# Optimization experiments

Measured on AMD Instinct MI355X. Metric: run time of the kernel, lower is better.

The kernel has to match this reference:

```python
import jax, jax.numpy as jnp
import numpy as np

N_NODES = 100000


def _gcn_layer(x, src, dst, W, b, num_nodes):
    # Linear transform first (PyG GCNConv applies Linear before propagate).
    h = x @ W.T  # [N, out]
    # Degree (with self loops already included in src/dst), computed on target.
    ones = jnp.ones(dst.shape[0], dtype=h.dtype)
    deg = jax.ops.segment_sum(ones, dst, num_segments=num_nodes)
    dinv = jnp.where(deg > 0, jax.lax.rsqrt(deg), 0.0)
    norm = dinv[src] * dinv[dst]  # [E]
    msg = h[src] * norm[:, None]  # gather + per-edge scale, [E, out]
    out = jax.ops.segment_sum(msg, dst, num_segments=num_nodes)
    return out + b


def setup_inputs() -> dict:
    key = jax.random.key(0)
    k1, k2, k3, k4, k5, k6 = jax.random.split(key, 6)
    d = 64
    x = jax.random.normal(k1, (N_NODES, d), dtype=jnp.float32)
    edge_index = jax.random.randint(k2, (2, 1600000), 0, N_NODES, dtype=jnp.int64)
    s = 1.0 / np.sqrt(d)
    W1 = jax.random.normal(k3, (d, d), dtype=jnp.float32) * s
    b1 = jax.random.normal(k4, (d,), dtype=jnp.float32) * 0.01
    W2 = jax.random.normal(k5, (d, d), dtype=jnp.float32) * s
    b2 = jax.random.normal(k6, (d,), dtype=jnp.float32) * 0.01
    return {"x": x, "edge_index": edge_index, "W1": W1, "b1": b1, "W2": W2, "b2": b2}


def reference(x, edge_index, W1, b1, W2, b2):
    n = x.shape[0]
    loop = jnp.arange(n, dtype=edge_index.dtype)
    src = jnp.concatenate([edge_index[0], loop])  # add self loops
    dst = jnp.concatenate([edge_index[1], loop])
    h = _gcn_layer(x, src, dst, W1, b1, n)
    out = _gcn_layer(h, src, dst, W2, b2, n)
    return out
```

## Files before the change

kernel.cpp:

```cpp
#include <hip/hip_runtime.h>
#include <hip/hip_fp16.h>


#define D 64
#define NPB 128
#define MAXB 784
#define CHUNK 8192

__global__ __launch_bounds__(256) void hist_kernel(const int* __restrict__ dst,
                                                   int* __restrict__ counts,
                                                   int* __restrict__ cursor,
                                                   int nE, int B) {
    __shared__ int hist[MAXB];
    if (blockIdx.x == 0 && threadIdx.x == 0) *cursor = 0;
    int c = blockIdx.x;
    for (int b = threadIdx.x; b < B; b += 256) hist[b] = 0;
    __syncthreads();
    int e0 = c * CHUNK;
#pragma unroll
    for (int i = 0; i < CHUNK / 256; ++i) {
        int e = e0 + i * 256 + threadIdx.x;
        if (e < nE) atomicAdd(&hist[dst[e] >> 7], 1);
    }
    __syncthreads();
    for (int b = threadIdx.x; b < B; b += 256) counts[c * B + b] = hist[b];
}

__global__ __launch_bounds__(256) void scan_alloc(int* __restrict__ counts,
                                                  int* __restrict__ btot,
                                                  int* __restrict__ bbase,
                                                  int* __restrict__ cursor,
                                                  int B, int C) {
    int b = blockIdx.x * 4 + (threadIdx.x >> 6);
    if (b >= B) return;
    int lane = threadIdx.x & 63;
    int running = 0;
    for (int c0 = 0; c0 < C; c0 += 64) {
        int c = c0 + lane;
        int v = (c < C) ? counts[c * B + b] : 0;
        int x = v;
#pragma unroll
        for (int s = 1; s < 64; s <<= 1) {
            int u = __shfl_up(x, s);
            if (lane >= s) x += u;
        }
        if (c < C) counts[c * B + b] = running + x - v;
        running += __shfl(x, 63);
    }
    if (lane == 0) {
        int base = atomicAdd(cursor, running);
        bbase[b] = base;
        btot[b]  = running;
    }
}

__global__ __launch_bounds__(256) void scatter0_kernel(const int* __restrict__ src,
                                                       const int* __restrict__ dst,
                                                       const int* __restrict__ base,
                                                       const int* __restrict__ bbase,
                                                       int* __restrict__ entries0,
                                                       int nE, int B) {
    __shared__ int cur[MAXB];
    int c = blockIdx.x;
    for (int b = threadIdx.x; b < B; b += 256) cur[b] = base[c * B + b] + bbase[b];
    __syncthreads();
    int e0 = c * CHUNK;
#pragma unroll
    for (int i = 0; i < CHUNK / 256; ++i) {
        int e = e0 + i * 256 + threadIdx.x;
        if (e < nE) {
            int s = src[e], d = dst[e];
            int pos = atomicAdd(&cur[d >> 7], 1);
            entries0[pos] = s | ((d & (NPB - 1)) << 17);
        }
    }
}

__global__ __launch_bounds__(256) void regroup_kernel(const int* __restrict__ entries0,
                                                      const int* __restrict__ bbase,
                                                      const int* __restrict__ btot,
                                                      int* __restrict__ off,
                                                      int* __restrict__ deg,
                                                      float* __restrict__ dinv,
                                                      int* __restrict__ entries1, int N) {
    __shared__ int cnt[NPB];
    __shared__ int scn[NPB];
    __shared__ int cur[NPB];
    int b = blockIdx.x;
    int t = threadIdx.x;
    if (t < NPB) cnt[t] = 0;
    __syncthreads();
    int s0 = bbase[b], s1 = s0 + btot[b];
    for (int p = s0 + t; p < s1; p += 256)
        atomicAdd(&cnt[(entries0[p] >> 17) & (NPB - 1)], 1);
    __syncthreads();
    if (t < NPB) scn[t] = cnt[t];
    __syncthreads();
    for (int s = 1; s < NPB; s <<= 1) {
        int u = 0;
        if (t < NPB && t >= s) u = scn[t - s];
        __syncthreads();
        if (t < NPB) scn[t] += u;
        __syncthreads();
    }
    if (t < NPB) {
        int node = b * NPB + t;
        int c = cnt[t];
        int o = s0 + scn[t] - c;
        cur[t] = o;
        if (node < N) {
            off[node]  = o;
            deg[node]  = c;
            dinv[node] = rsqrtf((float)c + 1.0f);
        }
    }
    __syncthreads();
    for (int p = s0 + t; p < s1; p += 256) {
        int e = entries0[p];
        int pos = atomicAdd(&cur[(e >> 17) & (NPB - 1)], 1);
        entries1[pos] = e & 0x1FFFF;
    }
}

template <typename OutT>
__global__ __launch_bounds__(256) void aggregate3(const int* __restrict__ csr,
                                                  const int* __restrict__ off,
                                                  const int* __restrict__ deg,
                                                  const float* __restrict__ dinv,
                                                  const __half* __restrict__ H,
                                                  const float* __restrict__ bias,
                                                  OutT* __restrict__ out, int N) {
    int node = blockIdx.x * 4 + (threadIdx.x >> 6);
    if (node >= N) return;
    int lane = threadIdx.x & 63;
    int p2 = lane & 31;
    int h  = lane >> 5;
    const __half2* H2 = (const __half2*)H;
    float dd = dinv[node];
    float2 acc = make_float2(0.0f, 0.0f);
    int beg = off[node];
    int end = beg + deg[node];
    int p = beg;
    for (; p + 16 <= end; p += 16) {
        int s[8];
#pragma unroll
        for (int i = 0; i < 8; ++i) s[i] = csr[p + 2 * i + h];
        __half2 g[8];
        float dv[8];
#pragma unroll
        for (int i = 0; i < 8; ++i) {
            g[i]  = H2[(size_t)s[i] * 32 + p2];
            dv[i] = dinv[s[i]];
        }
#pragma unroll
        for (int i = 0; i < 8; ++i) {
            float2 f = __half22float2(g[i]);
            float c = dv[i] * dd;
            acc.x += f.x * c; acc.y += f.y * c;
        }
    }
    for (; p + 8 <= end; p += 8) {
        int s0v = csr[p + 0 + h], s1v = csr[p + 2 + h];
        int s2v = csr[p + 4 + h], s3v = csr[p + 6 + h];
        __half2 g0 = H2[(size_t)s0v * 32 + p2];
        __half2 g1 = H2[(size_t)s1v * 32 + p2];
        __half2 g2 = H2[(size_t)s2v * 32 + p2];
        __half2 g3 = H2[(size_t)s3v * 32 + p2];
        float c0 = dinv[s0v] * dd, c1 = dinv[s1v] * dd;
        float c2 = dinv[s2v] * dd, c3 = dinv[s3v] * dd;
        float2 f0 = __half22float2(g0), f1 = __half22float2(g1);
        float2 f2 = __half22float2(g2), f3 = __half22float2(g3);
        acc.x += f0.x * c0; acc.y += f0.y * c0;
        acc.x += f1.x * c1; acc.y += f1.y * c1;
        acc.x += f2.x * c2; acc.y += f2.y * c2;
        acc.x += f3.x * c3; acc.y += f3.y * c3;
    }
    for (; p + 2 <= end; p += 2) {
        int s0v = csr[p + h];
        __half2 g0 = H2[(size_t)s0v * 32 + p2];
        float c0 = dinv[s0v] * dd;
        float2 f0 = __half22float2(g0);
        acc.x += f0.x * c0; acc.y += f0.y * c0;
    }
    if (p < end && h == 0) {
        int s0v = csr[p];
        __half2 g0 = H2[(size_t)s0v * 32 + p2];
        float c0 = dinv[s0v] * dd;
        float2 f0 = __half22float2(g0);
        acc.x += f0.x * c0; acc.y += f0.y * c0;
    }
    acc.x += __shfl_xor(acc.x, 32);
    acc.y += __shfl_xor(acc.y, 32);
    if (h == 0) {
        float s = dd * dd;
        float2 hs = __half22float2(H2[(size_t)node * 32 + p2]);
        float2 bv = ((const float2*)bias)[p2];
        float2 o;
        o.x = acc.x + bv.x + hs.x * s;
        o.y = acc.y + bv.y + hs.y * s;
        if constexpr (sizeof(OutT) == 2) {
            ((__half2*)(out + (size_t)node * D))[p2] = __float22half2_rn(o);
        } else {
            ((float2*)(out + (size_t)node * D))[p2] = o;
        }
    }
}

template <typename InT>
__global__ __launch_bounds__(256) void gemm_xwt_h(const InT* __restrict__ X,
                                                  const float* __restrict__ W,
                                                  __half* __restrict__ H, int N) {
    __shared__ float xt[64 * 68];
    __shared__ float wt[64 * 68];
    const int t = threadIdx.x;
    const int i0 = blockIdx.x * 64;
#pragma unroll
    for (int r = 0; r < 16; ++r) {
        int idx = r * 256 + t;
        int j = idx >> 6, k = idx & 63;
        wt[k * 68 + j] = W[idx];
    }
#pragma unroll
    for (int r = 0; r < 16; ++r) {
        int idx = r * 256 + t;
        int i = idx >> 6, k = idx & 63;
        float v = 0.0f;
        if (i0 + i < N) {
            if constexpr (sizeof(InT) == 2)
                v = __half2float(((const __half*)X)[(size_t)(i0 + i) * D + k]);
            else
                v = ((const float*)X)[(size_t)(i0 + i) * D + k];
        }
        xt[k * 68 + i] = v;
    }
    __syncthreads();
    const int tn = (t & 15) * 4;
    const int tc = (t >> 4) * 4;
    float acc[4][4] = {};
#pragma unroll 8
    for (int k = 0; k < 64; ++k) {
        const float4 xa = *(const float4*)(xt + k * 68 + tn);
        const float4 wb = *(const float4*)(wt + k * 68 + tc);
        acc[0][0] += xa.x * wb.x; acc[0][1] += xa.x * wb.y; acc[0][2] += xa.x * wb.z; acc[0][3] += xa.x * wb.w;
        acc[1][0] += xa.y * wb.x; acc[1][1] += xa.y * wb.y; acc[1][2] += xa.y * wb.z; acc[1][3] += xa.y * wb.w;
        acc[2][0] += xa.z * wb.x; acc[2][1] += xa.z * wb.y; acc[2][2] += xa.z * wb.z; acc[2][3] += xa.z * wb.w;
        acc[3][0] += xa.w * wb.x; acc[3][1] += xa.w * wb.y; acc[3][2] += xa.w * wb.z; acc[3][3] += xa.w * wb.w;
    }
#pragma unroll
    for (int a = 0; a < 4; ++a) {
        int i = i0 + tn + a;
        if (i < N) {
            union { __half2 h2[2]; uint2 u2; } pk;
            pk.h2[0].x = __float2half_rn(acc[a][0]);
            pk.h2[0].y = __float2half_rn(acc[a][1]);
            pk.h2[1].x = __float2half_rn(acc[a][2]);
            pk.h2[1].y = __float2half_rn(acc[a][3]);
            *(uint2*)(&H[(size_t)i * D + tc]) = pk.u2;
        }
    }
}

__global__ __launch_bounds__(256) void deg_kernel(const int* __restrict__ dst,
                                                  int* __restrict__ deg, int nE) {
    int e = blockIdx.x * 256 + threadIdx.x;
    if (e < nE) atomicAdd(&deg[dst[e]], 1);
}

__global__ __launch_bounds__(256) void dinv_kernel(const int* __restrict__ deg,
                                                   float* __restrict__ dinv, int N) {
    int i = blockIdx.x * 256 + threadIdx.x;
    if (i < N) dinv[i] = rsqrtf((float)deg[i] + 1.0f);
}

__global__ __launch_bounds__(256) void gemm_xwt(const float* __restrict__ X,
                                                const float* __restrict__ W,
                                                float* __restrict__ H, int N) {
    __shared__ float xt[64 * 68];
    __shared__ float wt[64 * 68];
    const int t = threadIdx.x;
    const int i0 = blockIdx.x * 64;
#pragma unroll
    for (int r = 0; r < 16; ++r) {
        int idx = r * 256 + t;
        int j = idx >> 6, k = idx & 63;
        wt[k * 68 + j] = W[idx];
    }
#pragma unroll
    for (int r = 0; r < 16; ++r) {
        int idx = r * 256 + t;
        int i = idx >> 6, k = idx & 63;
        float v = 0.0f;
        if (i0 + i < N) v = X[(size_t)(i0 + i) * D + k];
        xt[k * 68 + i] = v;
    }
    __syncthreads();
    const int tn = (t & 15) * 4;
    const int tc = (t >> 4) * 4;
    float acc[4][4] = {};
#pragma unroll 8
    for (int k = 0; k < 64; ++k) {
        const float4 xa = *(const float4*)(xt + k * 68 + tn);
        const float4 wb = *(const float4*)(wt + k * 68 + tc);
        acc[0][0] += xa.x * wb.x; acc[0][1] += xa.x * wb.y; acc[0][2] += xa.x * wb.z; acc[0][3] += xa.x * wb.w;
        acc[1][0] += xa.y * wb.x; acc[1][1] += xa.y * wb.y; acc[1][2] += xa.y * wb.z; acc[1][3] += xa.y * wb.w;
        acc[2][0] += xa.z * wb.x; acc[2][1] += xa.z * wb.y; acc[2][2] += xa.z * wb.z; acc[2][3] += xa.z * wb.w;
        acc[3][0] += xa.w * wb.x; acc[3][1] += xa.w * wb.y; acc[3][2] += xa.w * wb.z; acc[3][3] += xa.w * wb.w;
    }
#pragma unroll
    for (int a = 0; a < 4; ++a) {
        int i = i0 + tn + a;
        if (i < N) {
            float4 o = make_float4(acc[a][0], acc[a][1], acc[a][2], acc[a][3]);
            *(float4*)(H + (size_t)i * D + tc) = o;
        }
    }
}

__global__ __launch_bounds__(256) void init_out(const float* __restrict__ H,
                                                const float* __restrict__ dinv,
                                                const float* __restrict__ b,
                                                float* __restrict__ out, int N) {
    int idx4 = blockIdx.x * 256 + threadIdx.x;
    if (idx4 >= N * 16) return;
    int i = idx4 >> 4;
    int jc = idx4 & 15;
    float di = dinv[i];
    float s = di * di;
    float4 h4 = ((const float4*)H)[idx4];
    float4 b4 = ((const float4*)b)[jc];
    ((float4*)out)[idx4] = make_float4(b4.x + h4.x * s, b4.y + h4.y * s,
                                       b4.z + h4.z * s, b4.w + h4.w * s);
}

__global__ __launch_bounds__(256) void edge_scatter(const int* __restrict__ src,
                                                    const int* __restrict__ dst,
                                                    const float* __restrict__ dinv,
                                                    const float* __restrict__ H,
                                                    float* __restrict__ out, int nE) {
    int tid = blockIdx.x * 256 + threadIdx.x;
    int e = tid >> 4;
    if (e >= nE) return;
    int l = tid & 15;
    int s = src[e];
    int d = dst[e];
    float c = dinv[s] * dinv[d];
    float4 v = ((const float4*)H)[s * 16 + l];
    float* o = out + (size_t)d * D + l * 4;
    unsafeAtomicAdd(o + 0, v.x * c);
    unsafeAtomicAdd(o + 1, v.y * c);
    unsafeAtomicAdd(o + 2, v.z * c);
    unsafeAtomicAdd(o + 3, v.w * c);
}

static inline size_t align_up(size_t v, size_t a) { return (v + a - 1) & ~(a - 1); }

extern "C" void kernel_launch(void* const* d_in, const int* in_sizes, int n_in,
                              void* d_out, int out_size, void* d_ws, size_t ws_size,
                              hipStream_t stream) {
    const float* x  = (const float*)d_in[0];
    const int*   ei = (const int*)d_in[1];
    const float* W1 = (const float*)d_in[2];
    const float* b1 = (const float*)d_in[3];
    const float* W2 = (const float*)d_in[4];
    const float* b2 = (const float*)d_in[5];
    float* out = (float*)d_out;

    const int N  = in_sizes[0] / D;
    const int nE = in_sizes[1] / 2;
    const int* srcp = ei;
    const int* dstv = ei + nE;

    const int B = (N + NPB - 1) / NPB;
    const int C = (nE + CHUNK - 1) / CHUNK;

    char* base_p = (char*)d_ws;
    size_t o = 0;
    int* counts = (int*)(base_p + o);  o = align_up(o + (size_t)C * B * 4, 256);
    int* btot   = (int*)(base_p + o);  o = align_up(o + (size_t)B * 4, 256);
    int* bbase  = (int*)(base_p + o);  o = align_up(o + (size_t)B * 4, 256);
    int* cursor = (int*)(base_p + o);  o = align_up(o + 4, 256);
    int* off    = (int*)(base_p + o);  o = align_up(o + (size_t)N * 4, 256);
    int* deg    = (int*)(base_p + o);  o = align_up(o + (size_t)N * 4, 256);
    float* dinv = (float*)(base_p + o); o = align_up(o + (size_t)N * 4, 256);
    int* entries1 = (int*)(base_p + o); o = align_up(o + (size_t)nE * 4, 256);
    size_t r2 = (size_t)nE * 4 > (size_t)N * D * 2 ? (size_t)nE * 4 : (size_t)N * D * 2;
    int* entries0 = (int*)(base_p + o);
    __half* Hh    = (__half*)(base_p + o);
    o = align_up(o + r2, 256);
    size_t need_base = o;
    __half* A1h = (__half*)(base_p + o);
    size_t need_full = o + align_up((size_t)N * D * 2, 256);

    int gb_n = (N + 255) / 256;
    int gb_g = (N + 63) / 64;
    int gb_e = (nE + 255) / 256;

    if (ws_size >= need_base && B <= MAXB) {
        hist_kernel<<<C, 256, 0, stream>>>(dstv, counts, cursor, nE, B);
        scan_alloc<<<(B + 3) / 4, 256, 0, stream>>>(counts, btot, bbase, cursor, B, C);
        scatter0_kernel<<<C, 256, 0, stream>>>(srcp, dstv, counts, bbase, entries0, nE, B);
        regroup_kernel<<<B, 256, 0, stream>>>(entries0, bbase, btot, off, deg, dinv, entries1, N);

        int gb_a = (N + 3) / 4;
        gemm_xwt_h<float><<<gb_g, 256, 0, stream>>>(x, W1, Hh, N);
        if (ws_size >= need_full) {
            aggregate3<__half><<<gb_a, 256, 0, stream>>>(entries1, off, deg, dinv, Hh, b1, A1h, N);
            gemm_xwt_h<__half><<<gb_g, 256, 0, stream>>>(A1h, W2, Hh, N);
        } else {
            aggregate3<float><<<gb_a, 256, 0, stream>>>(entries1, off, deg, dinv, Hh, b1, out, N);
            gemm_xwt_h<float><<<gb_g, 256, 0, stream>>>(out, W2, Hh, N);
        }
        aggregate3<float><<<gb_a, 256, 0, stream>>>(entries1, off, deg, dinv, Hh, b2, out, N);
    } else {
        size_t fo = 0;
        int* fdeg    = (int*)(base_p + fo);  fo = align_up(fo + (size_t)N * 4, 256);
        float* fdinv = (float*)(base_p + fo); fo = align_up(fo + (size_t)N * 4, 256);
        float* bufA  = (float*)(base_p + fo);
        hipMemsetAsync(fdeg, 0, (size_t)N * 4, stream);
        deg_kernel<<<gb_e, 256, 0, stream>>>(dstv, fdeg, nE);
        dinv_kernel<<<gb_n, 256, 0, stream>>>(fdeg, fdinv, N);
        int gb_i = (N * 16 + 255) / 256;
        int gb_e16 = (int)(((long long)nE * 16 + 255) / 256);
        gemm_xwt<<<gb_g, 256, 0, stream>>>(x, W1, bufA, N);
        init_out<<<gb_i, 256, 0, stream>>>(bufA, fdinv, b1, out, N);
        edge_scatter<<<gb_e16, 256, 0, stream>>>(srcp, dstv, fdinv, bufA, out, nE);
        gemm_xwt<<<gb_g, 256, 0, stream>>>(out, W2, bufA, N);
        init_out<<<gb_i, 256, 0, stream>>>(bufA, fdinv, b2, out, N);
        edge_scatter<<<gb_e16, 256, 0, stream>>>(srcp, dstv, fdinv, bufA, out, nE);
    }
}
```

Baseline: 290.7 us.

## Fuse regroup with first GEMM, prescale layer-2 features by dinv, retune bucketing

The regroup (CSR build) kernel and the first feature GEMM now run as one launch, with blocks split by index, so the two independent stages overlap and one launch is dropped. The second GEMM multiplies each output row by dinv before storing, so the second aggregation can sum gathered rows without per-edge dinv loads and multiplies and applies dd once at the end. The histogram and scatter kernels move to 512-thread blocks with a smaller chunk. The workspace layout is rearranged into a new primary path plus a fallback path. Prescaling before the fp16 store changes rounding slightly.

```diff
diff --git a/kernel.cpp b/kernel.cpp
--- a/kernel.cpp
+++ b/kernel.cpp
@@ -5,25 +5,26 @@
 #define D 64
 #define NPB 128
 #define MAXB 784
-#define CHUNK 8192
-
-__global__ __launch_bounds__(256) void hist_kernel(const int* __restrict__ dst,
-                                                   int* __restrict__ counts,
-                                                   int* __restrict__ cursor,
-                                                   int nE, int B) {
+#define CHUNK 4096
+#define BT 512
+
+__global__ __launch_bounds__(BT) void hist_kernel(const int* __restrict__ dst,
+                                                  int* __restrict__ counts,
+                                                  int* __restrict__ cursor,
+                                                  int nE, int B) {
     __shared__ int hist[MAXB];
     if (blockIdx.x == 0 && threadIdx.x == 0) *cursor = 0;
     int c = blockIdx.x;
-    for (int b = threadIdx.x; b < B; b += 256) hist[b] = 0;
+    for (int b = threadIdx.x; b < B; b += BT) hist[b] = 0;
     __syncthreads();
     int e0 = c * CHUNK;
 #pragma unroll
-    for (int i = 0; i < CHUNK / 256; ++i) {
-        int e = e0 + i * 256 + threadIdx.x;
+    for (int i = 0; i < CHUNK / BT; ++i) {
+        int e = e0 + i * BT + threadIdx.x;
         if (e < nE) atomicAdd(&hist[dst[e] >> 7], 1);
     }
     __syncthreads();
-    for (int b = threadIdx.x; b < B; b += 256) counts[c * B + b] = hist[b];
+    for (int b = threadIdx.x; b < B; b += BT) counts[c * B + b] = hist[b];
 }
 
 __global__ __launch_bounds__(256) void scan_alloc(int* __restrict__ counts,
@@ -54,25 +55,68 @@
     }
 }
 
-__global__ __launch_bounds__(256) void scatter0_kernel(const int* __restrict__ src,
-                                                       const int* __restrict__ dst,
-                                                       const int* __restrict__ base,
-                                                       const int* __restrict__ bbase,
-                                                       int* __restrict__ entries0,
-                                                       int nE, int B) {
+__global__ __launch_bounds__(BT) void scatter0_kernel(const int* __restrict__ src,
+                                                      const int* __restrict__ dst,
+                                                      const int* __restrict__ base,
+                                                      const int* __restrict__ bbase,
+                                                      int* __restrict__ entries0,
+                                                      int nE, int B) {
     __shared__ int cur[MAXB];
     int c = blockIdx.x;
-    for (int b = threadIdx.x; b < B; b += 256) cur[b] = base[c * B + b] + bbase[b];
+    for (int b = threadIdx.x; b < B; b += BT) cur[b] = base[c * B + b] + bbase[b];
     __syncthreads();
     int e0 = c * CHUNK;
 #pragma unroll
-    for (int i = 0; i < CHUNK / 256; ++i) {
-        int e = e0 + i * 256 + threadIdx.x;
+    for (int i = 0; i < CHUNK / BT; ++i) {
+        int e = e0 + i * BT + threadIdx.x;
         if (e < nE) {
             int s = src[e], d = dst[e];
             int pos = atomicAdd(&cur[d >> 7], 1);
             entries0[pos] = s | ((d & (NPB - 1)) << 17);
         }
+    }
+}
+
+__device__ __forceinline__ void regroup_body(const int* __restrict__ entries0,
+                                             const int* __restrict__ bbase,
+                                             const int* __restrict__ btot,
+                                             int* __restrict__ off,
+                                             int* __restrict__ deg,
+                                             float* __restrict__ dinv,
+                                             int* __restrict__ entries1, int N, int b,
+                                             int* cnt, int* scn, int* cur) {
+    int t = threadIdx.x;
+    if (t < NPB) cnt[t] = 0;
+    __syncthreads();
+    int s0 = bbase[b], s1 = s0 + btot[b];
+    for (int p = s0 + t; p < s1; p += 256)
+        atomicAdd(&cnt[(entries0[p] >> 17) & (NPB - 1)], 1);
+    __syncthreads();
+    if (t < NPB) scn[t] = cnt[t];
+    __syncthreads();
+    for (int s = 1; s < NPB; s <<= 1) {
+        int u = 0;
+        if (t < NPB && t >= s) u = scn[t - s];
+        __syncthreads();
+        if (t < NPB) scn[t] += u;
+        __syncthreads();
+    }
+    if (t < NPB) {
+        int node = b * NPB + t;
+        int c = cnt[t];
+        int o = s0 + scn[t] - c;
+        cur[t] = o;
+        if (node < N) {
+            off[node]  = o;
+            deg[node]  = c;
+            dinv[node] = rsqrtf((float)c + 1.0f);
+        }
+    }
+    __syncthreads();
+    for (int p = s0 + t; p < s1; p += 256) {
+        int e = entries0[p];
+        int pos = atomicAdd(&cur[(e >> 17) & (NPB - 1)], 1);
+        entries1[pos] = e & 0x1FFFF;
     }
 }
 
@@ -86,43 +130,99 @@
     __shared__ int cnt[NPB];
     __shared__ int scn[NPB];
     __shared__ int cur[NPB];
-    int b = blockIdx.x;
-    int t = threadIdx.x;
-    if (t < NPB) cnt[t] = 0;
-    __syncthreads();
-    int s0 = bbase[b], s1 = s0 + btot[b];
-    for (int p = s0 + t; p < s1; p += 256)
-        atomicAdd(&cnt[(entries0[p] >> 17) & (NPB - 1)], 1);
-    __syncthreads();
-    if (t < NPB) scn[t] = cnt[t];
-    __syncthreads();
-    for (int s = 1; s < NPB; s <<= 1) {
-        int u = 0;
-        if (t < NPB && t >= s) u = scn[t - s];
-        __syncthreads();
-        if (t < NPB) scn[t] += u;
-        __syncthreads();
-    }
-    if (t < NPB) {
-        int node = b * NPB + t;
-        int c = cnt[t];
-        int o = s0 + scn[t] - c;
-        cur[t] = o;
-        if (node < N) {
-            off[node]  = o;
-            deg[node]  = c;
-            dinv[node] = rsqrtf((float)c + 1.0f);
-        }
-    }
-    __syncthreads();
-    for (int p = s0 + t; p < s1; p += 256) {
-        int e = entries0[p];
-        int pos = atomicAdd(&cur[(e >> 17) & (NPB - 1)], 1);
-        entries1[pos] = e & 0x1FFFF;
-    }
-}
-
-template <typename OutT>
+    regroup_body(entries0, bbase, btot, off, deg, dinv, entries1, N, blockIdx.x,
+                 cnt, scn, cur);
+}
+
+template <typename InT>
+__device__ __forceinline__ void gemm_body(const InT* __restrict__ X,
+                                          const float* __restrict__ W,
+                                          const float* __restrict__ scale,
+                                          __half* __restrict__ H, int N, int bx,
+                                          float* xt, float* wt) {
+    const int t = threadIdx.x;
+    const int i0 = bx * 64;
+#pragma unroll
+    for (int r = 0; r < 16; ++r) {
+        int idx = r * 256 + t;
+        int j = idx >> 6, k = idx & 63;
+        wt[k * 68 + j] = W[idx];
+    }
+#pragma unroll
+    for (int r = 0; r < 16; ++r) {
+        int idx = r * 256 + t;
+        int i = idx >> 6, k = idx & 63;
+        float v = 0.0f;
+        if (i0 + i < N) {
+            if constexpr (sizeof(InT) == 2)
+                v = __half2float(((const __half*)X)[(size_t)(i0 + i) * D + k]);
+            else
+                v = ((const float*)X)[(size_t)(i0 + i) * D + k];
+        }
+        xt[k * 68 + i] = v;
+    }
+    __syncthreads();
+    const int tn = (t & 15) * 4;
+    const int tc = (t >> 4) * 4;
+    float acc[4][4] = {};
+#pragma unroll 8
+    for (int k = 0; k < 64; ++k) {
+        const float4 xa = *(const float4*)(xt + k * 68 + tn);
+        const float4 wb = *(const float4*)(wt + k * 68 + tc);
+        acc[0][0] += xa.x * wb.x; acc[0][1] += xa.x * wb.y; acc[0][2] += xa.x * wb.z; acc[0][3] += xa.x * wb.w;
+        acc[1][0] += xa.y * wb.x; acc[1][1] += xa.y * wb.y; acc[1][2] += xa.y * wb.z; acc[1][3] += xa.y * wb.w;
+        acc[2][0] += xa.z * wb.x; acc[2][1] += xa.z * wb.y; acc[2][2] += xa.z * wb.z; acc[2][3] += xa.z * wb.w;
+        acc[3][0] += xa.w * wb.x; acc[3][1] += xa.w * wb.y; acc[3][2] += xa.w * wb.z; acc[3][3] += xa.w * wb.w;
+    }
+#pragma unroll
+    for (int a = 0; a < 4; ++a) {
+        int i = i0 + tn + a;
+        if (i < N) {
+            float sc = scale ? scale[i] : 1.0f;
+            union { __half2 h2[2]; uint2 u2; } pk;
+            pk.h2[0].x = __float2half_rn(acc[a][0] * sc);
+            pk.h2[0].y = __float2half_rn(acc[a][1] * sc);
+            pk.h2[1].x = __float2half_rn(acc[a][2] * sc);
+            pk.h2[1].y = __float2half_rn(acc[a][3] * sc);
+            *(uint2*)(&H[(size_t)i * D + tc]) = pk.u2;
+        }
+    }
+}
+
+template <typename InT>
+__global__ __launch_bounds__(256) void gemm_xwt_h(const InT* __restrict__ X,
+                                                  const float* __restrict__ W,
+                                                  const float* __restrict__ scale,
+                                                  __half* __restrict__ H, int N) {
+    __shared__ float xt[64 * 68];
+    __shared__ float wt[64 * 68];
+    gemm_body<InT>(X, W, scale, H, N, blockIdx.x, xt, wt);
+}
+
+__global__ __launch_bounds__(256) void regroup_gemm1(const int* __restrict__ entries0,
+                                                     const int* __restrict__ bbase,
+                                                     const int* __restrict__ btot,
+                                                     int* __restrict__ off,
+                                                     int* __restrict__ deg,
+                                                     float* __restrict__ dinv,
+                                                     int* __restrict__ entries1, int N, int B,
+                                                     const float* __restrict__ X,
+                                                     const float* __restrict__ W1,
+                                                     __half* __restrict__ Hh) {
+    __shared__ float xt[64 * 68];
+    __shared__ float wt[64 * 68];
+    if ((int)blockIdx.x < B) {
+        int* cnt = (int*)xt;
+        int* scn = cnt + NPB;
+        int* cur = scn + NPB;
+        regroup_body(entries0, bbase, btot, off, deg, dinv, entries1, N,
+                     blockIdx.x, cnt, scn, cur);
+    } else {
+        gemm_body<float>(X, W1, nullptr, Hh, N, (int)blockIdx.x - B, xt, wt);
+    }
+}
+
+template <typename OutT, bool PRESCALED>
 __global__ __launch_bounds__(256) void aggregate3(const int* __restrict__ csr,
                                                   const int* __restrict__ off,
                                                   const int* __restrict__ deg,
@@ -146,17 +246,24 @@
 #pragma unroll
         for (int i = 0; i < 8; ++i) s[i] = csr[p + 2 * i + h];
         __half2 g[8];
-        float dv[8];
-#pragma unroll
-        for (int i = 0; i < 8; ++i) {
-            g[i]  = H2[(size_t)s[i] * 32 + p2];
-            dv[i] = dinv[s[i]];
-        }
-#pragma unroll
-        for (int i = 0; i < 8; ++i) {
-            float2 f = __half22float2(g[i]);
-            float c = dv[i] * dd;
-            acc.x += f.x * c; acc.y += f.y * c;
+#pragma unroll
+        for (int i = 0; i < 8; ++i) g[i] = H2[(size_t)s[i] * 32 + p2];
+        if constexpr (PRESCALED) {
+#pragma unroll
+            for (int i = 0; i < 8; ++i) {
+                float2 f = __half22float2(g[i]);
+                acc.x += f.x; acc.y += f.y;
+            }
+        } else {
+            float dv[8];
+#pragma unroll
+            for (int i = 0; i < 8; ++i) dv[i] = dinv[s[i]];
+#pragma unroll
+            for (int i = 0; i < 8; ++i) {
+                float2 f = __half22float2(g[i]);
+                float c = dv[i] * dd;
+                acc.x += f.x * c; acc.y += f.y * c;
+            }
         }
     }
     for (; p + 8 <= end; p += 8) {
@@ -166,96 +273,60 @@
         __half2 g1 = H2[(size_t)s1v * 32 + p2];
         __half2 g2 = H2[(size_t)s2v * 32 + p2];
         __half2 g3 = H2[(size_t)s3v * 32 + p2];
-        float c0 = dinv[s0v] * dd, c1 = dinv[s1v] * dd;
-        float c2 = dinv[s2v] * dd, c3 = dinv[s3v] * dd;
         float2 f0 = __half22float2(g0), f1 = __half22float2(g1);
         float2 f2 = __half22float2(g2), f3 = __half22float2(g3);
-        acc.x += f0.x * c0; acc.y += f0.y * c0;
-        acc.x += f1.x * c1; acc.y += f1.y * c1;
-        acc.x += f2.x * c2; acc.y += f2.y * c2;
-        acc.x += f3.x * c3; acc.y += f3.y * c3;
+        if constexpr (PRESCALED) {
+            acc.x += f0.x + f1.x + f2.x + f3.x;
+            acc.y += f0.y + f1.y + f2.y + f3.y;
+        } else {
+            float c0 = dinv[s0v] * dd, c1 = dinv[s1v] * dd;
+            float c2 = dinv[s2v] * dd, c3 = dinv[s3v] * dd;
+            acc.x += f0.x * c0; acc.y += f0.y * c0;
+            acc.x += f1.x * c1; acc.y += f1.y * c1;
+            acc.x += f2.x * c2; acc.y += f2.y * c2;
+            acc.x += f3.x * c3; acc.y += f3.y * c3;
+        }
     }
     for (; p + 2 <= end; p += 2) {
         int s0v = csr[p + h];
         __half2 g0 = H2[(size_t)s0v * 32 + p2];
-        float c0 = dinv[s0v] * dd;
         float2 f0 = __half22float2(g0);
-        acc.x += f0.x * c0; acc.y += f0.y * c0;
+        if constexpr (PRESCALED) {
+            acc.x += f0.x; acc.y += f0.y;
+        } else {
+            float c0 = dinv[s0v] * dd;
+            acc.x += f0.x * c0; acc.y += f0.y * c0;
+        }
     }
     if (p < end && h == 0) {
         int s0v = csr[p];
         __half2 g0 = H2[(size_t)s0v * 32 + p2];
-        float c0 = dinv[s0v] * dd;
         float2 f0 = __half22float2(g0);
-        acc.x += f0.x * c0; acc.y += f0.y * c0;
+        if constexpr (PRESCALED) {
+            acc.x += f0.x; acc.y += f0.y;
+        } else {
+            float c0 = dinv[s0v] * dd;
+            acc.x += f0.x * c0; acc.y += f0.y * c0;
+        }
     }
     acc.x += __shfl_xor(acc.x, 32);
     acc.y += __shfl_xor(acc.y, 32);
     if (h == 0) {
-        float s = dd * dd;
         float2 hs = __half22float2(H2[(size_t)node * 32 + p2]);
         float2 bv = ((const float2*)bias)[p2];
         float2 o;
-        o.x = acc.x + bv.x + hs.x * s;
-        o.y = acc.y + bv.y + hs.y * s;
+        if constexpr (PRESCALED) {
+            o.x = (acc.x + hs.x) * dd + bv.x;
+            o.y = (acc.y + hs.y) * dd + bv.y;
+        } else {
+            float s = dd * dd;
+            o.x = acc.x + bv.x + hs.x * s;
+            o.y = acc.y + bv.y + hs.y * s;
+        }
         if constexpr (sizeof(OutT) == 2) {
             ((__half2*)(out + (size_t)node * D))[p2] = __float22half2_rn(o);
         } else {
             ((float2*)(out + (size_t)node * D))[p2] = o;
-        }
-    }
-}
-
-template <typename InT>
-__global__ __launch_bounds__(256) void gemm_xwt_h(const InT* __restrict__ X,
-                                                  const float* __restrict__ W,
-                                                  __half* __restrict__ H, int N) {
-    __shared__ float xt[64 * 68];
-    __shared__ float wt[64 * 68];
-    const int t = threadIdx.x;
-    const int i0 = blockIdx.x * 64;
-#pragma unroll
-    for (int r = 0; r < 16; ++r) {
-        int idx = r * 256 + t;
-        int j = idx >> 6, k = idx & 63;
-        wt[k * 68 + j] = W[idx];
-    }
-#pragma unroll
-    for (int r = 0; r < 16; ++r) {
-        int idx = r * 256 + t;
-        int i = idx >> 6, k = idx & 63;
-        float v = 0.0f;
-        if (i0 + i < N) {
-            if constexpr (sizeof(InT) == 2)
-                v = __half2float(((const __half*)X)[(size_t)(i0 + i) * D + k]);
-            else
-                v = ((const float*)X)[(size_t)(i0 + i) * D + k];
-        }
-        xt[k * 68 + i] = v;
-    }
-    __syncthreads();
-    const int tn = (t & 15) * 4;
-    const int tc = (t >> 4) * 4;
-    float acc[4][4] = {};
-#pragma unroll 8
-    for (int k = 0; k < 64; ++k) {
-        const float4 xa = *(const float4*)(xt + k * 68 + tn);
-        const float4 wb = *(const float4*)(wt + k * 68 + tc);
-        acc[0][0] += xa.x * wb.x; acc[0][1] += xa.x * wb.y; acc[0][2] += xa.x * wb.z; acc[0][3] += xa.x * wb.w;
-        acc[1][0] += xa.y * wb.x; acc[1][1] += xa.y * wb.y; acc[1][2] += xa.y * wb.z; acc[1][3] += xa.y * wb.w;
-        acc[2][0] += xa.z * wb.x; acc[2][1] += xa.z * wb.y; acc[2][2] += xa.z * wb.z; acc[2][3] += xa.z * wb.w;
-        acc[3][0] += xa.w * wb.x; acc[3][1] += xa.w * wb.y; acc[3][2] += xa.w * wb.z; acc[3][3] += xa.w * wb.w;
-    }
-#pragma unroll
-    for (int a = 0; a < 4; ++a) {
-        int i = i0 + tn + a;
-        if (i < N) {
-            union { __half2 h2[2]; uint2 u2; } pk;
-            pk.h2[0].x = __float2half_rn(acc[a][0]);
-            pk.h2[0].y = __float2half_rn(acc[a][1]);
-            pk.h2[1].x = __float2half_rn(acc[a][2]);
-            pk.h2[1].y = __float2half_rn(acc[a][3]);
-            *(uint2*)(&H[(size_t)i * D + tc]) = pk.u2;
         }
     }
 }
@@ -374,6 +445,12 @@
     const int C = (nE + CHUNK - 1) / CHUNK;
 
     char* base_p = (char*)d_ws;
+
+    int gb_n = (N + 255) / 256;
+    int gb_g = (N + 63) / 64;
+    int gb_e = (nE + 255) / 256;
+    int gb_a = (N + 3) / 4;
+
     size_t o = 0;
     int* counts = (int*)(base_p + o);  o = align_up(o + (size_t)C * B * 4, 256);
     int* btot   = (int*)(base_p + o);  o = align_up(o + (size_t)B * 4, 256);
@@ -383,34 +460,58 @@
     int* deg    = (int*)(base_p + o);  o = align_up(o + (size_t)N * 4, 256);
     float* dinv = (float*)(base_p + o); o = align_up(o + (size_t)N * 4, 256);
     int* entries1 = (int*)(base_p + o); o = align_up(o + (size_t)nE * 4, 256);
-    size_t r2 = (size_t)nE * 4 > (size_t)N * D * 2 ? (size_t)nE * 4 : (size_t)N * D * 2;
+    size_t rX = (size_t)nE * 4 > (size_t)N * D * 2 ? (size_t)nE * 4 : (size_t)N * D * 2;
     int* entries0 = (int*)(base_p + o);
+    __half* A1h   = (__half*)(base_p + o);
+    o = align_up(o + rX, 256);
     __half* Hh    = (__half*)(base_p + o);
-    o = align_up(o + r2, 256);
-    size_t need_base = o;
-    __half* A1h = (__half*)(base_p + o);
-    size_t need_full = o + align_up((size_t)N * D * 2, 256);
-
-    int gb_n = (N + 255) / 256;
-    int gb_g = (N + 63) / 64;
-    int gb_e = (nE + 255) / 256;
-
-    if (ws_size >= need_base && B <= MAXB) {
-        hist_kernel<<<C, 256, 0, stream>>>(dstv, counts, cursor, nE, B);
+    size_t need1 = o + align_up((size_t)N * D * 2, 256);
+
+    size_t o2 = 0;
+    int* counts2 = (int*)(base_p + o2);  o2 = align_up(o2 + (size_t)C * B * 4, 256);
+    int* btot2   = (int*)(base_p + o2);  o2 = align_up(o2 + (size_t)B * 4, 256);
+    int* bbase2  = (int*)(base_p + o2);  o2 = align_up(o2 + (size_t)B * 4, 256);
+    int* cursor2 = (int*)(base_p + o2);  o2 = align_up(o2 + 4, 256);
+    int* off2    = (int*)(base_p + o2);  o2 = align_up(o2 + (size_t)N * 4, 256);
+    int* deg2    = (int*)(base_p + o2);  o2 = align_up(o2 + (size_t)N * 4, 256);
+    float* dinv2 = (float*)(base_p + o2); o2 = align_up(o2 + (size_t)N * 4, 256);
+    int* entries1b = (int*)(base_p + o2); o2 = align_up(o2 + (size_t)nE * 4, 256);
+    int* entries0b = (int*)(base_p + o2);
+    __half* Hh2    = (__half*)(base_p + o2);
+    o2 = align_up(o2 + rX, 256);
+    size_t need_base = o2;
+    __half* A1h2 = (__half*)(base_p + o2);
+    size_t need_full = o2 + align_up((size_t)N * D * 2, 256);
+
+    if (ws_size >= need1 && B <= MAXB) {
+        hist_kernel<<<C, BT, 0, stream>>>(dstv, counts, cursor, nE, B);
         scan_alloc<<<(B + 3) / 4, 256, 0, stream>>>(counts, btot, bbase, cursor, B, C);
-        scatter0_kernel<<<C, 256, 0, stream>>>(srcp, dstv, counts, bbase, entries0, nE, B);
-        regroup_kernel<<<B, 256, 0, stream>>>(entries0, bbase, btot, off, deg, dinv, entries1, N);
-
-        int gb_a = (N + 3) / 4;
-        gemm_xwt_h<float><<<gb_g, 256, 0, stream>>>(x, W1, Hh, N);
+        scatter0_kernel<<<C, BT, 0, stream>>>(srcp, dstv, counts, bbase, entries0, nE, B);
+        regroup_gemm1<<<B + gb_g, 256, 0, stream>>>(entries0, bbase, btot, off, deg,
+                                                    dinv, entries1, N, B, x, W1, Hh);
+        aggregate3<__half, false><<<gb_a, 256, 0, stream>>>(entries1, off, deg, dinv,
+                                                            Hh, b1, A1h, N);
+        gemm_xwt_h<__half><<<gb_g, 256, 0, stream>>>(A1h, W2, dinv, Hh, N);
+        aggregate3<float, true><<<gb_a, 256, 0, stream>>>(entries1, off, deg, dinv,
+                                                          Hh, b2, out, N);
+    } else if (ws_size >= need_base && B <= MAXB) {
+        hist_kernel<<<C, BT, 0, stream>>>(dstv, counts2, cursor2, nE, B);
+        scan_alloc<<<(B + 3) / 4, 256, 0, stream>>>(counts2, btot2, bbase2, cursor2, B, C);
+        scatter0_kernel<<<C, BT, 0, stream>>>(srcp, dstv, counts2, bbase2, entries0b, nE, B);
+        regroup_kernel<<<B, 256, 0, stream>>>(entries0b, bbase2, btot2, off2, deg2,
+                                              dinv2, entries1b, N);
+        gemm_xwt_h<float><<<gb_g, 256, 0, stream>>>(x, W1, nullptr, Hh2, N);
         if (ws_size >= need_full) {
-            aggregate3<__half><<<gb_a, 256, 0, stream>>>(entries1, off, deg, dinv, Hh, b1, A1h, N);
-            gemm_xwt_h<__half><<<gb_g, 256, 0, stream>>>(A1h, W2, Hh, N);
-        } else {
-            aggregate3<float><<<gb_a, 256, 0, stream>>>(entries1, off, deg, dinv, Hh, b1, out, N);
-            gemm_xwt_h<float><<<gb_g, 256, 0, stream>>>(out, W2, Hh, N);
-        }
-        aggregate3<float><<<gb_a, 256, 0, stream>>>(entries1, off, deg, dinv, Hh, b2, out, N);
+            aggregate3<__half, false><<<gb_a, 256, 0, stream>>>(entries1b, off2, deg2,
+                                                                dinv2, Hh2, b1, A1h2, N);
+            gemm_xwt_h<__half><<<gb_g, 256, 0, stream>>>(A1h2, W2, dinv2, Hh2, N);
+        } else {
+            aggregate3<float, false><<<gb_a, 256, 0, stream>>>(entries1b, off2, deg2,
+                                                               dinv2, Hh2, b1, out, N);
+            gemm_xwt_h<float><<<gb_g, 256, 0, stream>>>(out, W2, dinv2, Hh2, N);
+        }
+        aggregate3<float, true><<<gb_a, 256, 0, stream>>>(entries1b, off2, deg2, dinv2,
+                                                          Hh2, b2, out, N);
     } else {
         size_t fo = 0;
         int* fdeg    = (int*)(base_p + fo);  fo = align_up(fo + (size_t)N * 4, 256);
```

Result: faster. 276.0 us (-5.1%).
